# Kernel tuning notes

Hardware: AMD Instinct MI355X
Metric: run time of the kernel (lower is better)

The kernel has to match this reference:

```python
import jax, jax.numpy as jnp
import numpy as np

N, E = 20000, 100000
D_IN, H1, C1 = 512, 8, 64   # conv1: 512 -> 8 heads x 64, concat -> 512
H2, C2 = 4, 128             # conv2: 512 -> 4 heads x 128, mean -> 128


def setup_inputs() -> dict:
    key = jax.random.key(0)
    k = jax.random.split(key, 12)
    s_in = 1.0 / np.sqrt(D_IN).astype(np.float32)
    return {
        "street_embedding": jax.random.normal(k[0], (N, D_IN), jnp.float32),
        "edge_index": jax.random.randint(k[1], (2, E), 0, N),
        "y": jax.random.randint(k[2], (N,), 0, C2),
        "train_mask": jax.random.bernoulli(k[3], 0.5, (N,)),
        "W1": jax.random.normal(k[4], (D_IN, H1 * C1), jnp.float32) * s_in,
        "att_src1": jax.random.normal(k[5], (H1, C1), jnp.float32) * 0.1,
        "att_dst1": jax.random.normal(k[6], (H1, C1), jnp.float32) * 0.1,
        "b1": jnp.zeros((H1 * C1,), jnp.float32),
        "W2": jax.random.normal(k[7], (H1 * C1, H2 * C2), jnp.float32) * s_in,
        "att_src2": jax.random.normal(k[8], (H2, C2), jnp.float32) * 0.1,
        "att_dst2": jax.random.normal(k[9], (H2, C2), jnp.float32) * 0.1,
        "b2": jnp.zeros((C2,), jnp.float32),
    }


def _gat_conv(x, W, a_src, a_dst, b, src, dst, n, H, C, concat):
    # linear transform (no bias, as in PyG GATConv's internal lin)
    xp = (x @ W).reshape(n, H, C)                      # [N,H,C]
    asrc = jnp.einsum('nhc,hc->nh', xp, a_src)         # [N,H]
    adst = jnp.einsum('nhc,hc->nh', xp, a_dst)
    e = jax.nn.leaky_relu(asrc[src] + adst[dst], 0.2)  # [E',H] edge scores
    # softmax over incoming edges per destination node
    m = jax.lax.stop_gradient(jax.ops.segment_max(e, dst, num_segments=n))
    ex = jnp.exp(e - m[dst])
    denom = jax.ops.segment_sum(ex, dst, num_segments=n)
    alpha = ex / (denom[dst] + 1e-16)                  # [E',H]
    out = jax.ops.segment_sum(alpha[:, :, None] * xp[src], dst, num_segments=n)  # [N,H,C]
    if concat:
        return out.reshape(n, H * C) + b
    return out.mean(axis=1) + b


def reference(street_embedding, edge_index, y, train_mask,
              W1, att_src1, att_dst1, b1, W2, att_src2, att_dst2, b2):
    n = street_embedding.shape[0]
    loop = jnp.arange(n)
    # PyG GATConv adds self-loops by default
    src = jnp.concatenate([edge_index[0], loop])
    dst = jnp.concatenate([edge_index[1], loop])
    # dropout layers are identity in eval mode
    h = _gat_conv(street_embedding, W1, att_src1, att_dst1, b1, src, dst, n, H1, C1, True)
    h = jax.nn.elu(h)
    out = _gat_conv(h, W2, att_src2, att_dst2, b2, src, dst, n, H2, C2, False)  # [N,C2]
    # CrossEntropyLoss, mean over train_mask nodes (weighted mean, jit-safe)
    logp = jax.nn.log_softmax(out, axis=-1)
    ce = -jnp.take_along_axis(logp, y[:, None], axis=-1)[:, 0]
    w = train_mask.astype(out.dtype)
    loss_su = jnp.sum(w * ce) / jnp.sum(w)
    return (loss_su, out)
```

## Files before the change

### kernel.cpp

```cpp
#include <hip/hip_runtime.h>
#include <cmath>

#define D_IN 512
#define HC   512
#define NH1  8
#define NC1  64
#define NH2  4
#define NC2  128
#define BM 128
#define BN 128

typedef __attribute__((ext_vector_type(8))) short short8;
typedef __attribute__((ext_vector_type(8))) unsigned short u16x8;
typedef __attribute__((ext_vector_type(4))) float f32x4;

__device__ inline ushort f2bf(float f) {
  unsigned u = __float_as_uint(f);
  return (ushort)((u + 0x7FFFu + ((u >> 16) & 1u)) >> 16);
}
__device__ inline float bf2f(ushort b) { return __uint_as_float(((unsigned)b) << 16); }

__global__ void k_cast_all(const float* __restrict__ x, ushort* __restrict__ Abf,
                           const float* __restrict__ W1, const float* __restrict__ W2,
                           ushort* __restrict__ Wt1, ushort* __restrict__ Wt2, int n4x) {
  const int KN = D_IN * HC;
  int i = blockIdx.x * blockDim.x + threadIdx.x;
  if (i < n4x) {
    float4 v = ((const float4*)x)[i];
    ushort4 r = { f2bf(v.x), f2bf(v.y), f2bf(v.z), f2bf(v.w) };
    ((ushort4*)Abf)[i] = r;
  } else {
    int idx = i - n4x;
    if (idx >= 2 * KN) return;
    const float* W = (idx < KN) ? W1 : W2;
    ushort* Wt = (idx < KN) ? Wt1 : Wt2;
    int j = (idx < KN) ? idx : idx - KN;
    int n = j / D_IN, k = j - n * D_IN;
    Wt[j] = f2bf(W[(size_t)k * HC + n]);
  }
}

template<int H>
__global__ void k_gemm_bf16(const ushort* __restrict__ A, const ushort* __restrict__ Bt,
                            ushort* __restrict__ Cbf,
                            const float* __restrict__ att_s, const float* __restrict__ att_d,
                            float* __restrict__ asrc, float* __restrict__ adst, int M) {
  constexpr int C = HC / H;
  __shared__ __align__(16) ushort As[2 * 4096];
  __shared__ __align__(16) ushort Bs[2 * 4096];
  int t = threadIdx.x;

  int nwg = gridDim.x * gridDim.y;
  int lin = blockIdx.y * gridDim.x + blockIdx.x;
  int q = nwg >> 3, r = nwg & 7;
  int xcd = lin & 7, pos = lin >> 3;
  int wg = (xcd < r ? xcd * (q + 1) : r * (q + 1) + (xcd - r) * q) + pos;
  int m0 = (wg >> 2) * BM;
  int n0 = (wg & 3) * BN;

  int wave = t >> 6, lane = t & 63;
  int ln = lane & 15, qd = lane >> 4;
  int wm = (wave >> 1) * 64, wn = (wave & 1) * 64;

  f32x4 acc[4][4] = {};

  int g = t >> 6, ct = (t >> 4) & 3, lt = t & 15;
  int rA0 = m0 + g * 16 + lt;      if (rA0 > M - 1) rA0 = M - 1;
  int rA1 = m0 + 64 + g * 16 + lt; if (rA1 > M - 1) rA1 = M - 1;
  const ushort* gA0 = A + (size_t)rA0 * D_IN + ct * 8;
  const ushort* gA1 = A + (size_t)rA1 * D_IN + ct * 8;
  const ushort* gB0 = Bt + (size_t)(n0 + g * 16 + lt) * D_IN + ct * 8;
  const ushort* gB1 = Bt + (size_t)(n0 + 64 + g * 16 + lt) * D_IN + ct * 8;

#define STAGE(buf, ko)                                                          \
  do {                                                                          \
    int lo_ = (buf) * 4096;                                                     \
    __builtin_amdgcn_global_load_lds(                                           \
        (const __attribute__((address_space(1))) void*)(gA0 + (ko)),            \
        (__attribute__((address_space(3))) void*)(As + lo_ + t * 8), 16, 0, 0); \
    __builtin_amdgcn_global_load_lds(                                           \
        (const __attribute__((address_space(1))) void*)(gA1 + (ko)),            \
        (__attribute__((address_space(3))) void*)(As + lo_ + 2048 + t * 8), 16, 0, 0); \
    __builtin_amdgcn_global_load_lds(                                           \
        (const __attribute__((address_space(1))) void*)(gB0 + (ko)),            \
        (__attribute__((address_space(3))) void*)(Bs + lo_ + t * 8), 16, 0, 0); \
    __builtin_amdgcn_global_load_lds(                                           \
        (const __attribute__((address_space(1))) void*)(gB1 + (ko)),            \
        (__attribute__((address_space(3))) void*)(Bs + lo_ + 2048 + t * 8), 16, 0, 0); \
  } while (0)

  STAGE(0, 0);
  int cur = 0;
  for (int it = 0; it < 16; ++it) {
    if (it < 15) {
      STAGE(cur ^ 1, (it + 1) * 32);
      asm volatile("s_waitcnt vmcnt(4)" ::: "memory");
    } else {
      asm volatile("s_waitcnt vmcnt(0)" ::: "memory");
    }
    __builtin_amdgcn_s_barrier();
    int lo = cur * 4096;
    short8 a[4], bb[4];
#pragma unroll
    for (int i = 0; i < 4; ++i)
      a[i] = *(const short8*)&As[lo + (((wave >> 1) * 4 + i) * 4 + qd) * 128 + ln * 8];
#pragma unroll
    for (int j = 0; j < 4; ++j)
      bb[j] = *(const short8*)&Bs[lo + (((wave & 1) * 4 + j) * 4 + qd) * 128 + ln * 8];
#pragma unroll
    for (int i = 0; i < 4; ++i)
#pragma unroll
      for (int j = 0; j < 4; ++j)
        acc[i][j] = __builtin_amdgcn_mfma_f32_16x16x32_bf16(a[i], bb[j], acc[i][j], 0, 0, 0);
    __builtin_amdgcn_s_barrier();
    cur ^= 1;
  }
#undef STAGE

#pragma unroll
  for (int i = 0; i < 4; ++i) {
#pragma unroll
    for (int reg = 0; reg < 4; ++reg) {
      int row = m0 + wm + i * 16 + qd * 4 + reg;
      if (row >= M) continue;
#pragma unroll
      for (int j = 0; j < 4; ++j)
        Cbf[(size_t)row * HC + n0 + wn + j * 16 + ln] = f2bf(acc[i][j][reg]);
    }
  }

  int colbase = n0 + wn;
  int h = colbase / C;
  float sa[4], da[4];
#pragma unroll
  for (int j = 0; j < 4; ++j) {
    int c = (colbase % C) + j * 16 + ln;
    sa[j] = att_s[h * C + c];
    da[j] = att_d[h * C + c];
  }
#pragma unroll
  for (int i = 0; i < 4; ++i) {
#pragma unroll
    for (int reg = 0; reg < 4; ++reg) {
      float ps = acc[i][0][reg] * sa[0] + acc[i][1][reg] * sa[1]
               + acc[i][2][reg] * sa[2] + acc[i][3][reg] * sa[3];
      float pd = acc[i][0][reg] * da[0] + acc[i][1][reg] * da[1]
               + acc[i][2][reg] * da[2] + acc[i][3][reg] * da[3];
#pragma unroll
      for (int o = 1; o < 16; o <<= 1) { ps += __shfl_xor(ps, o); pd += __shfl_xor(pd, o); }
      int row = m0 + wm + i * 16 + qd * 4 + reg;
      if (ln == 0 && row < M) {
        if (C == 64) {
          asrc[row * H + h] = ps; adst[row * H + h] = pd;
        } else {
          int sub = (colbase >> 6) & 1;
          asrc[(row * H + h) * 2 + sub] = ps;
          adst[(row * H + h) * 2 + sub] = pd;
        }
      }
    }
  }
}

__global__ void k_hist(const int* __restrict__ ei, int E, int Etot, int* __restrict__ cnt) {
  int e = blockIdx.x * blockDim.x + threadIdx.x;
  if (e >= Etot) return;
  int d = (e < E) ? ei[E + e] : e - E;
  atomicAdd(&cnt[d], 1);
}

__global__ void k_scan(const int* __restrict__ cnt, int* __restrict__ rowstart, int N) {
  int tid = threadIdx.x;
  int T = (N + 1023) / 1024;
  int base = tid * T;
  int sum = 0;
  for (int i = 0; i < T; ++i) { int j = base + i; if (j < N) sum += cnt[j]; }
  int lane = tid & 63, w = tid >> 6;
  int v = sum;
#pragma unroll
  for (int off = 1; off < 64; off <<= 1) {
    int u = __shfl_up(v, off);
    if (lane >= off) v += u;
  }
  __shared__ int wsum[16];
  if (lane == 63) wsum[w] = v;
  __syncthreads();
  if (tid < 16) {
    int tv = wsum[tid];
#pragma unroll
    for (int off = 1; off < 16; off <<= 1) {
      int u = __shfl_up(tv, off);
      if (tid >= off) tv += u;
    }
    wsum[tid] = tv;
  }
  __syncthreads();
  int wave_prefix = (w == 0) ? 0 : wsum[w - 1];
  int run = wave_prefix + v - sum;
  for (int i = 0; i < T; ++i) {
    int j = base + i;
    if (j < N) { rowstart[j] = run; run += cnt[j]; }
  }
  if (tid == 1023) rowstart[N] = run;
}

__global__ void k_scatter(const int* __restrict__ ei, int E, int Etot,
                          const int* __restrict__ rowstart, int* __restrict__ cursor,
                          int* __restrict__ csr_src) {
  int e = blockIdx.x * blockDim.x + threadIdx.x;
  if (e >= Etot) return;
  int s = (e < E) ? ei[e] : e - E;
  int d = (e < E) ? ei[E + e] : e - E;
  int pos = atomicAdd(&cursor[d], 1);
  csr_src[rowstart[d] + pos] = s;
}

template<int H, int MODE>
__global__ void k_agg(const int* __restrict__ rowstart, const int* __restrict__ csr_src,
                      const float* __restrict__ asrc, const float* __restrict__ adst,
                      const ushort* __restrict__ xp, ushort* __restrict__ hout,
                      float* __restrict__ out2, const float* __restrict__ bias,
                      const int* __restrict__ y, const int* __restrict__ msk,
                      float* __restrict__ acc2, int N) {
  constexpr int C = HC / H;
  int wv = threadIdx.x >> 6, lane = threadIdx.x & 63;
  int n = blockIdx.x * 4 + wv;
  if (n >= N) return;
  int h = (MODE == 1) ? (lane >> 3) : (lane >> 4);
  int beg = rowstart[n], end = rowstart[n + 1];

  float adn;
  if (MODE == 1) adn = adst[n * H + h];
  else { float2 t2 = ((const float2*)adst)[n * H + h]; adn = t2.x + t2.y; }

  float acc[8] = {};
  float wsum = 0.f;

  for (int c0 = beg; c0 < end; c0 += 64) {
    int len = end - c0; if (len > 64) len = 64;
    int ev = (lane < len) ? csr_src[c0 + lane] : 0;
    int j = 0;
    for (; j + 1 < len; j += 2) {
      int s0 = __shfl(ev, j), s1 = __shfl(ev, j + 1);
      float v0, v1;
      if (MODE == 1) { v0 = asrc[s0 * H + h]; v1 = asrc[s1 * H + h]; }
      else {
        float2 p0 = ((const float2*)asrc)[s0 * H + h];
        float2 p1 = ((const float2*)asrc)[s1 * H + h];
        v0 = p0.x + p0.y; v1 = p1.x + p1.y;
      }
      u16x8 a0 = ((const u16x8*)xp)[(size_t)s0 * 64 + lane];
      u16x8 a1 = ((const u16x8*)xp)[(size_t)s1 * 64 + lane];
      v0 += adn; v1 += adn;
      v0 = (v0 > 0.f) ? v0 : 0.2f * v0;
      v1 = (v1 > 0.f) ? v1 : 0.2f * v1;
      float w0 = __expf(v0), w1 = __expf(v1);
#pragma unroll
      for (int k = 0; k < 8; ++k)
        acc[k] += w0 * bf2f(a0[k]) + w1 * bf2f(a1[k]);
      wsum += w0 + w1;
    }
    if (j < len) {
      int s0 = __shfl(ev, j);
      float v0;
      if (MODE == 1) v0 = asrc[s0 * H + h];
      else { float2 p0 = ((const float2*)asrc)[s0 * H + h]; v0 = p0.x + p0.y; }
      u16x8 a0 = ((const u16x8*)xp)[(size_t)s0 * 64 + lane];
      v0 += adn;
      v0 = (v0 > 0.f) ? v0 : 0.2f * v0;
      float w0 = __expf(v0);
#pragma unroll
      for (int k = 0; k < 8; ++k) acc[k] += w0 * bf2f(a0[k]);
      wsum += w0;
    }
  }
  float rdn = 1.0f / (wsum + 1e-16f);
#pragma unroll
  for (int k = 0; k < 8; ++k) acc[k] *= rdn;

  if (MODE == 1) {
    int c = lane * 8;
    u16x8 rr;
#pragma unroll
    for (int k = 0; k < 8; ++k) {
      float v = acc[k] + bias[c + k];
      v = (v > 0.f) ? v : expm1f(v);
      rr[k] = f2bf(v);
    }
    ((u16x8*)hout)[(size_t)n * 64 + lane] = rr;
  } else {
#pragma unroll
    for (int k = 0; k < 8; ++k) {
      float v = acc[k];
      v += __shfl_xor(v, 16);
      v += __shfl_xor(v, 32);
      acc[k] = v * 0.25f + bias[(lane & 15) * 8 + k];
    }
    if (lane < 16) {
      int cb = lane * 8;
#pragma unroll
      for (int k = 0; k < 8; ++k) out2[(size_t)n * NC2 + cb + k] = acc[k];
    }
    float mx = acc[0];
#pragma unroll
    for (int k = 1; k < 8; ++k) mx = fmaxf(mx, acc[k]);
#pragma unroll
    for (int o = 1; o < 16; o <<= 1) mx = fmaxf(mx, __shfl_xor(mx, o));
    float e = 0.f;
#pragma unroll
    for (int k = 0; k < 8; ++k) e += __expf(acc[k] - mx);
#pragma unroll
    for (int o = 1; o < 16; o <<= 1) e += __shfl_xor(e, o);
    int yv = y[n];
    float sel = acc[0];
#pragma unroll
    for (int k = 1; k < 8; ++k) sel = ((yv & 7) == k) ? acc[k] : sel;
    float vy = __shfl(sel, yv >> 3);
    if (lane == 0 && msk[n] != 0) {
      float ce = mx + logf(e) - vy;
      int slot = n & 127;
      atomicAdd(&acc2[slot], ce);
      atomicAdd(&acc2[128 + slot], 1.0f);
    }
  }
}

__global__ void k_final(const float* __restrict__ acc2, float* __restrict__ out0) {
  int tid = threadIdx.x;
  float ce = acc2[tid], ct = acc2[128 + tid];
#pragma unroll
  for (int o = 32; o > 0; o >>= 1) { ce += __shfl_xor(ce, o); ct += __shfl_xor(ct, o); }
  __shared__ float s[4];
  if ((tid & 63) == 0) { s[(tid >> 6) * 2] = ce; s[(tid >> 6) * 2 + 1] = ct; }
  __syncthreads();
  if (tid == 0) out0[0] = (s[0] + s[2]) / (s[1] + s[3]);
}

extern "C" void kernel_launch(void* const* d_in, const int* in_sizes, int n_in,
                              void* d_out, int out_size, void* d_ws, size_t ws_size,
                              hipStream_t stream) {
  const float* x   = (const float*)d_in[0];
  const int*   ei  = (const int*)d_in[1];
  const int*   y   = (const int*)d_in[2];
  const int*   msk = (const int*)d_in[3];
  const float* W1  = (const float*)d_in[4];
  const float* as1 = (const float*)d_in[5];
  const float* ad1 = (const float*)d_in[6];
  const float* b1  = (const float*)d_in[7];
  const float* W2  = (const float*)d_in[8];
  const float* as2 = (const float*)d_in[9];
  const float* ad2 = (const float*)d_in[10];
  const float* b2  = (const float*)d_in[11];
  float* out = (float*)d_out;

  int N = in_sizes[0] / D_IN;
  int E = in_sizes[1] / 2;
  int Etot = E + N;

  float* ws = (float*)d_ws;
  size_t NF = (size_t)N * HC;
  float* asr1 = ws;
  float* adt1 = asr1 + (size_t)N * NH1;
  float* asr2 = adt1 + (size_t)N * NH1;
  float* adt2 = asr2 + (size_t)N * 2 * NH2;
  float* acc2 = adt2 + (size_t)N * 2 * NH2;
  int*   cnt    = (int*)(acc2 + 256);
  int*   cursor = cnt + N;
  size_t zero_bytes = (256 + 2 * (size_t)N) * sizeof(float);
  int*   rowstart = cursor + N;
  int*   csr_src  = rowstart + N + 1;
  ushort* xpbf = (ushort*)((((uintptr_t)(csr_src + Etot)) + 15) & ~(uintptr_t)15);
  ushort* Abf = xpbf + NF;
  ushort* Wt1 = Abf + NF;
  ushort* Wt2 = Wt1 + (size_t)D_IN * HC;

  hipMemsetAsync(acc2, 0, zero_bytes, stream);

  int n4x = (int)(NF / 4);
  int cast_total = n4x + 2 * D_IN * HC;
  k_cast_all<<<(cast_total + 255) / 256, 256, 0, stream>>>(x, Abf, W1, W2, Wt1, Wt2, n4x);

  k_hist<<<(Etot + 255) / 256, 256, 0, stream>>>(ei, E, Etot, cnt);
  k_scan<<<1, 1024, 0, stream>>>(cnt, rowstart, N);
  k_scatter<<<(Etot + 255) / 256, 256, 0, stream>>>(ei, E, Etot, rowstart, cursor, csr_src);

  dim3 ggrid(HC / BN, (N + BM - 1) / BM);
  int aggblocks = (N + 3) / 4;

  k_gemm_bf16<NH1><<<ggrid, 256, 0, stream>>>(Abf, Wt1, xpbf, as1, ad1, asr1, adt1, N);
  k_agg<NH1, 1><<<aggblocks, 256, 0, stream>>>(rowstart, csr_src, asr1, adt1, xpbf, Abf,
                                               nullptr, b1, nullptr, nullptr, nullptr, N);

  k_gemm_bf16<NH2><<<ggrid, 256, 0, stream>>>(Abf, Wt2, xpbf, as2, ad2, asr2, adt2, N);
  k_agg<NH2, 2><<<aggblocks, 256, 0, stream>>>(rowstart, csr_src, asr2, adt2, xpbf, nullptr,
                                               out + 1, b2, y, msk, acc2, N);

  k_final<<<1, 128, 0, stream>>>(acc2, out);
}
```

Baseline: 296.0 us.

## Triple-buffer GEMM LDS staging and fuse edge histogram into cast kernel

The bf16 GEMM moves from double to triple-buffered LDS staging, keeping two K-tiles of global→LDS loads in flight ahead of the MFMA compute, with a peeled tail. This aims to hide global load latency better, at the cost of 48KB of LDS per block, which may reduce occupancy. Separately, the destination-degree histogram is folded into the cast/transpose kernel to remove one launch.

```diff
diff --git a/kernel.cpp b/kernel.cpp
--- a/kernel.cpp
+++ b/kernel.cpp
@@ -20,23 +20,29 @@
 }
 __device__ inline float bf2f(ushort b) { return __uint_as_float(((unsigned)b) << 16); }
 
-__global__ void k_cast_all(const float* __restrict__ x, ushort* __restrict__ Abf,
-                           const float* __restrict__ W1, const float* __restrict__ W2,
-                           ushort* __restrict__ Wt1, ushort* __restrict__ Wt2, int n4x) {
+__global__ void k_pre(const float* __restrict__ x, ushort* __restrict__ Abf,
+                      const float* __restrict__ W1, const float* __restrict__ W2,
+                      ushort* __restrict__ Wt1, ushort* __restrict__ Wt2, int n4x,
+                      const int* __restrict__ ei, int E, int Etot,
+                      int* __restrict__ cnt) {
   const int KN = D_IN * HC;
   int i = blockIdx.x * blockDim.x + threadIdx.x;
   if (i < n4x) {
     float4 v = ((const float4*)x)[i];
     ushort4 r = { f2bf(v.x), f2bf(v.y), f2bf(v.z), f2bf(v.w) };
     ((ushort4*)Abf)[i] = r;
-  } else {
+  } else if (i < n4x + 2 * KN) {
     int idx = i - n4x;
-    if (idx >= 2 * KN) return;
     const float* W = (idx < KN) ? W1 : W2;
     ushort* Wt = (idx < KN) ? Wt1 : Wt2;
     int j = (idx < KN) ? idx : idx - KN;
     int n = j / D_IN, k = j - n * D_IN;
     Wt[j] = f2bf(W[(size_t)k * HC + n]);
+  } else {
+    int e = i - n4x - 2 * KN;
+    if (e >= Etot) return;
+    int d = (e < E) ? ei[E + e] : e - E;
+    atomicAdd(&cnt[d], 1);
   }
 }
 
@@ -46,8 +52,8 @@
                             const float* __restrict__ att_s, const float* __restrict__ att_d,
                             float* __restrict__ asrc, float* __restrict__ adst, int M) {
   constexpr int C = HC / H;
-  __shared__ __align__(16) ushort As[2 * 4096];
-  __shared__ __align__(16) ushort Bs[2 * 4096];
+  __shared__ __align__(16) ushort As[3 * 4096];
+  __shared__ __align__(16) ushort Bs[3 * 4096];
   int t = threadIdx.x;
 
   int nwg = gridDim.x * gridDim.y;
@@ -89,33 +95,44 @@
         (__attribute__((address_space(3))) void*)(Bs + lo_ + 2048 + t * 8), 16, 0, 0); \
   } while (0)
 
+#define COMPUTE(BUF)                                                            \
+  do {                                                                          \
+    int lo = (BUF) * 4096;                                                      \
+    short8 a[4], bb[4];                                                         \
+    _Pragma("unroll") for (int i = 0; i < 4; ++i)                               \
+      a[i] = *(const short8*)&As[lo + (((wave >> 1) * 4 + i) * 4 + qd) * 128 + ln * 8]; \
+    _Pragma("unroll") for (int j = 0; j < 4; ++j)                               \
+      bb[j] = *(const short8*)&Bs[lo + (((wave & 1) * 4 + j) * 4 + qd) * 128 + ln * 8]; \
+    _Pragma("unroll") for (int i = 0; i < 4; ++i)                               \
+      _Pragma("unroll") for (int j = 0; j < 4; ++j)                             \
+        acc[i][j] = __builtin_amdgcn_mfma_f32_16x16x32_bf16(a[i], bb[j], acc[i][j], 0, 0, 0); \
+  } while (0)
+
   STAGE(0, 0);
-  int cur = 0;
-  for (int it = 0; it < 16; ++it) {
-    if (it < 15) {
-      STAGE(cur ^ 1, (it + 1) * 32);
-      asm volatile("s_waitcnt vmcnt(4)" ::: "memory");
-    } else {
-      asm volatile("s_waitcnt vmcnt(0)" ::: "memory");
-    }
+  STAGE(1, 32);
+  int cb = 0;
+  for (int it = 0; it < 14; ++it) {
+    int sb = (it + 2) % 3;
+    STAGE(sb, (it + 2) * 32);
+    asm volatile("s_waitcnt vmcnt(8)" ::: "memory");
     __builtin_amdgcn_s_barrier();
-    int lo = cur * 4096;
-    short8 a[4], bb[4];
-#pragma unroll
-    for (int i = 0; i < 4; ++i)
-      a[i] = *(const short8*)&As[lo + (((wave >> 1) * 4 + i) * 4 + qd) * 128 + ln * 8];
-#pragma unroll
-    for (int j = 0; j < 4; ++j)
-      bb[j] = *(const short8*)&Bs[lo + (((wave & 1) * 4 + j) * 4 + qd) * 128 + ln * 8];
-#pragma unroll
-    for (int i = 0; i < 4; ++i)
-#pragma unroll
-      for (int j = 0; j < 4; ++j)
-        acc[i][j] = __builtin_amdgcn_mfma_f32_16x16x32_bf16(a[i], bb[j], acc[i][j], 0, 0, 0);
+    asm volatile("" ::: "memory");
+    COMPUTE(cb);
+    asm volatile("" ::: "memory");
     __builtin_amdgcn_s_barrier();
-    cur ^= 1;
-  }
+    asm volatile("" ::: "memory");
+    cb = (cb == 2) ? 0 : cb + 1;
+  }
+  asm volatile("s_waitcnt vmcnt(4)" ::: "memory");
+  __builtin_amdgcn_s_barrier();
+  asm volatile("" ::: "memory");
+  COMPUTE(2);
+  asm volatile("s_waitcnt vmcnt(0)" ::: "memory");
+  __builtin_amdgcn_s_barrier();
+  asm volatile("" ::: "memory");
+  COMPUTE(0);
 #undef STAGE
+#undef COMPUTE
 
 #pragma unroll
   for (int i = 0; i < 4; ++i) {
@@ -160,13 +177,6 @@
       }
     }
   }
-}
-
-__global__ void k_hist(const int* __restrict__ ei, int E, int Etot, int* __restrict__ cnt) {
-  int e = blockIdx.x * blockDim.x + threadIdx.x;
-  if (e >= Etot) return;
-  int d = (e < E) ? ei[E + e] : e - E;
-  atomicAdd(&cnt[d], 1);
 }
 
 __global__ void k_scan(const int* __restrict__ cnt, int* __restrict__ rowstart, int N) {
@@ -377,10 +387,10 @@
   hipMemsetAsync(acc2, 0, zero_bytes, stream);
 
   int n4x = (int)(NF / 4);
-  int cast_total = n4x + 2 * D_IN * HC;
-  k_cast_all<<<(cast_total + 255) / 256, 256, 0, stream>>>(x, Abf, W1, W2, Wt1, Wt2, n4x);
-
-  k_hist<<<(Etot + 255) / 256, 256, 0, stream>>>(ei, E, Etot, cnt);
+  int pre_total = n4x + 2 * D_IN * HC + Etot;
+  k_pre<<<(pre_total + 255) / 256, 256, 0, stream>>>(x, Abf, W1, W2, Wt1, Wt2, n4x,
+                                                     ei, E, Etot, cnt);
+
   k_scan<<<1, 1024, 0, stream>>>(cnt, rowstart, N);
   k_scatter<<<(Etot + 255) / 256, 256, 0, stream>>>(ei, E, Etot, rowstart, cursor, csr_src);
 
```

Result: no change. 294.4 us (-0.5%).
